# Optimization experiments

Measured on AMD Instinct MI355X. Metric: run time of the kernel, lower is better.

The kernel has to match this reference:

```python
import jax, jax.numpy as jnp
import numpy as np

N_NODES = 50000
N_EDGES = 800000
D_IN = 128
D_OUT = 128


def setup_inputs() -> dict:
    key = jax.random.key(0)
    k1, k2, k3, k4 = jax.random.split(key, 4)
    node_features = jax.random.normal(k1, (N_NODES, D_IN), dtype=jnp.float32)
    edge_index = jax.random.randint(k2, (2, N_EDGES), 0, N_NODES, dtype=jnp.int64)
    # nn.Linear params: weight [out, in], bias [out]
    W = jax.random.normal(k3, (D_OUT, D_IN), dtype=jnp.float32) / np.sqrt(D_IN)
    b = jax.random.normal(k4, (D_OUT,), dtype=jnp.float32) * 0.01
    return {"node_features": node_features, "edge_index": edge_index, "W": W, "b": b}


def reference(node_features, edge_index, W, b):
    source_nodes = edge_index[0]
    dest_nodes = edge_index[1]
    # gather neighbor features [E, D_in], scatter-add into [N, D_in]
    neighbor_features = node_features[source_nodes]
    aggregated = jax.ops.segment_sum(neighbor_features, dest_nodes,
                                     num_segments=node_features.shape[0])
    # nn.Linear: x @ W.T + b
    return aggregated @ W.T + b
```

## Files before the change

### kernel.cpp

```cpp
#include <hip/hip_runtime.h>


constexpr int NN = 50000;
constexpr int NE = 800000;
constexpr int D  = 128;

constexpr int BS   = 128;
constexpr int NB   = (NN + BS - 1) / BS;
constexpr int EPB  = 4096;
constexpr int NSB  = (NE + EPB - 1) / EPB;
constexpr int CAP  = 4096;

constexpr int AROWU = 136;

typedef __attribute__((ext_vector_type(8))) short bf16x8;
typedef __attribute__((ext_vector_type(4))) float f32x4;
typedef __attribute__((ext_vector_type(2))) float f32x2;

__device__ inline unsigned short f2bf(float f) {
    unsigned u = __float_as_uint(f);
    return (unsigned short)((u + 0x7fffu + ((u >> 16) & 1u)) >> 16);
}
__device__ inline float bflo(unsigned v) { return __uint_as_float(v << 16); }
__device__ inline float bfhi(unsigned v) { return __uint_as_float(v & 0xffff0000u); }

__device__ inline int wscan(int v) {
    #pragma unroll
    for (int o = 1; o < 64; o <<= 1) {
        int u = __shfl_up(v, o);
        if ((int)(threadIdx.x & 63) >= o) v += u;
    }
    return v;
}

__device__ inline void acc8(f32x2& a0, f32x2& a1, f32x2& a2, f32x2& a3, uint4 v) {
    a0 += (f32x2){bflo(v.x), bfhi(v.x)};
    a1 += (f32x2){bflo(v.y), bfhi(v.y)};
    a2 += (f32x2){bflo(v.z), bfhi(v.z)};
    a3 += (f32x2){bflo(v.w), bfhi(v.w)};
}

constexpr int NF4 = NN * D / 4;
constexpr int W4  = D * D / 4;
constexpr int NBLK_P = (NF4 + W4 + 511) / 512;
constexpr int GRID_A = NSB + NBLK_P;

__global__ __launch_bounds__(512) void k_prep_bucket(
    const float* __restrict__ nf, const float* __restrict__ W,
    const int* __restrict__ ei,
    ushort* __restrict__ nfh, ushort* __restrict__ Wh,
    ushort* __restrict__ offs, unsigned* __restrict__ buf)
{
    __shared__ int hist[NB], cur[NB];
    __shared__ int wsum[8];
    __shared__ unsigned spk[EPB];
    const int t = threadIdx.x, lane = t & 63, w = t >> 6;

    if (blockIdx.x < NSB) {
        const int blk = blockIdx.x;
        const int e0  = blk * EPB;
        int cnt = NE - e0; if (cnt > EPB) cnt = EPB;

        for (int i = t; i < NB; i += 512) hist[i] = 0;
        __syncthreads();

        unsigned pk[8];
        #pragma unroll
        for (int j = 0; j < 8; ++j) {
            int idx = j * 512 + t;
            if (idx < cnt) {
                int e = e0 + idx;
                unsigned s = (unsigned)ei[e];
                unsigned d = (unsigned)ei[NE + e];
                pk[j] = (d << 16) | s;
                atomicAdd(&hist[pk[j] >> 23], 1);
            }
        }
        __syncthreads();
        int h = (t < NB) ? hist[t] : 0;
        int v = wscan(h);
        if (lane == 63) wsum[w] = v;
        __syncthreads();
        int addv = 0;
        #pragma unroll
        for (int i = 0; i < 8; ++i) addv += (i < w) ? wsum[i] : 0;
        v += addv;
        if (t < NB) {
            int ex = v - h;
            cur[t] = ex;
            offs[t * NSB + blk] = (ushort)ex;
        }
        if (t == 0) offs[NB * NSB + blk] = (ushort)cnt;
        __syncthreads();
        #pragma unroll
        for (int j = 0; j < 8; ++j) {
            int idx = j * 512 + t;
            if (idx < cnt) {
                int l = atomicAdd(&cur[pk[j] >> 23], 1);
                spk[l] = pk[j];
            }
        }
        __syncthreads();
        for (int i = t; i < cnt; i += 512)
            buf[(size_t)blk * EPB + i] = spk[i];
    } else {
        int i = (blockIdx.x - NSB) * 512 + t;
        if (i < NF4) {
            float4 v = ((const float4*)nf)[i];
            ((ushort4*)nfh)[i] = make_ushort4(f2bf(v.x), f2bf(v.y), f2bf(v.z), f2bf(v.w));
        } else if (i < NF4 + W4) {
            int k = i - NF4;
            float4 v = ((const float4*)W)[k];
            ((ushort4*)Wh)[k] = make_ushort4(f2bf(v.x), f2bf(v.y), f2bf(v.z), f2bf(v.w));
        }
    }
}

__global__ __launch_bounds__(1024, 8) void k_sort_agg(
    const unsigned* __restrict__ nfh, const unsigned* __restrict__ buf,
    const ushort* __restrict__ offs, const ushort* __restrict__ Wh,
    const float* __restrict__ bias, float* __restrict__ out)
{
    __shared__ ushort srt[CAP];
    __shared__ int scnt[256];
    __shared__ int sbase[NSB], rbase[NSB];
    __shared__ int hist[BS], off[BS], cur[BS];
    __shared__ int wred[16];
    __shared__ __align__(16) unsigned tile[BS * AROWU / 2];
    const int b = blockIdx.x, t = threadIdx.x;
    const int lane = t & 63, w = t >> 6;

    int my = 0;
    if (t < NSB) {
        int o0 = (int)offs[b * NSB + t];
        int o1 = (int)offs[(b + 1) * NSB + t];
        rbase[t] = o0;
        my = o1 - o0;
    }
    if (t < BS) hist[t] = 0;
    int vs = 0;
    if (w < 4) {
        vs = wscan(my);
        if (lane == 63) wred[w] = vs;
    }
    __syncthreads();
    if (w < 4) {
        int addv = 0;
        #pragma unroll
        for (int i = 0; i < 3; ++i) addv += (i < w) ? wred[i] : 0;
        vs += addv;
        scnt[t] = vs;
        if (t < NSB) sbase[t] = vs - my;
    }
    __syncthreads();
    int total = scnt[NSB - 1];
    if (total > CAP) total = CAP;

    unsigned mypk[4];
    int mycnt = 0;
    #pragma unroll
    for (int j = 0; j < 4; ++j) {
        int p = t + j * 1024;
        if (p < total) {
            int lo = 0, hi = NSB - 1;
            while (lo < hi) {
                int mid = (lo + hi) >> 1;
                if (scnt[mid] > p) hi = mid; else lo = mid + 1;
            }
            unsigned pk = buf[(size_t)lo * EPB + rbase[lo] + (p - sbase[lo])];
            mypk[j] = pk;
            atomicAdd(&hist[(pk >> 16) & (BS - 1)], 1);
            mycnt = j + 1;
        }
    }
    __syncthreads();

    int hv = (t < BS) ? hist[t] : 0;
    int nv = 0;
    if (w < 2) {
        nv = wscan(hv);
        if (lane == 63) wred[8 + w] = nv;
    }
    __syncthreads();
    if (t < BS) {
        int ex = nv + ((w == 1) ? wred[8] : 0) - hv;
        off[t] = ex; cur[t] = ex;
    }
    __syncthreads();
    #pragma unroll
    for (int j = 0; j < 4; ++j) {
        if (j < mycnt) {
            unsigned pk = mypk[j];
            int n = (pk >> 16) & (BS - 1);
            int p = atomicAdd(&cur[n], 1);
            srt[p] = (ushort)(pk & 0xffffu);
        }
    }
    __syncthreads();

    const int qq = lane >> 4;
    const int sl = lane & 15;
    const uint4* nfv = (const uint4*)nfh;

    #pragma unroll 1
    for (int i = 0; i < 2; ++i) {
        const int n = w * 8 + i * 4 + qq;
        const int beg = off[n], cnt = hist[n];
        f32x2 a0 = {0.f, 0.f}, a1 = {0.f, 0.f}, a2 = {0.f, 0.f}, a3 = {0.f, 0.f};
        const int nfull = cnt & ~3;
        if (nfull > 0) {
            uint4 v0 = nfv[(size_t)srt[beg + 0] * 16 + sl];
            uint4 v1 = nfv[(size_t)srt[beg + 1] * 16 + sl];
            uint4 v2 = nfv[(size_t)srt[beg + 2] * 16 + sl];
            uint4 v3 = nfv[(size_t)srt[beg + 3] * 16 + sl];
            for (int p = 4; p < nfull; p += 4) {
                uint4 u0 = nfv[(size_t)srt[beg + p + 0] * 16 + sl];
                uint4 u1 = nfv[(size_t)srt[beg + p + 1] * 16 + sl];
                uint4 u2 = nfv[(size_t)srt[beg + p + 2] * 16 + sl];
                uint4 u3 = nfv[(size_t)srt[beg + p + 3] * 16 + sl];
                acc8(a0, a1, a2, a3, v0);
                acc8(a0, a1, a2, a3, v1);
                acc8(a0, a1, a2, a3, v2);
                acc8(a0, a1, a2, a3, v3);
                v0 = u0; v1 = u1; v2 = u2; v3 = u3;
            }
            acc8(a0, a1, a2, a3, v0);
            acc8(a0, a1, a2, a3, v1);
            acc8(a0, a1, a2, a3, v2);
            acc8(a0, a1, a2, a3, v3);
        }
        const int r = cnt - nfull;
        uint4 t0, t1, t2;
        if (r > 0) t0 = nfv[(size_t)srt[beg + nfull + 0] * 16 + sl];
        if (r > 1) t1 = nfv[(size_t)srt[beg + nfull + 1] * 16 + sl];
        if (r > 2) t2 = nfv[(size_t)srt[beg + nfull + 2] * 16 + sl];
        if (r > 0) acc8(a0, a1, a2, a3, t0);
        if (r > 1) acc8(a0, a1, a2, a3, t1);
        if (r > 2) acc8(a0, a1, a2, a3, t2);

        uint4 o;
        o.x = (unsigned)f2bf(a0.x) | ((unsigned)f2bf(a0.y) << 16);
        o.y = (unsigned)f2bf(a1.x) | ((unsigned)f2bf(a1.y) << 16);
        o.z = (unsigned)f2bf(a2.x) | ((unsigned)f2bf(a2.y) << 16);
        o.w = (unsigned)f2bf(a3.x) | ((unsigned)f2bf(a3.y) << 16);
        *(uint4*)(tile + n * (AROWU / 2) + sl * 4) = o;
    }
    __syncthreads();

    const int m = lane & 15, q = lane >> 4;
    const ushort* lds = (const ushort*)tile;
    #pragma unroll
    for (int i = 0; i < 4; ++i) {
        const int task = w + 16 * i;
        const int t16  = task >> 3;
        const int c0   = (task & 7) * 16;
        const int grow0 = b * BS + t16 * 16;
        if (grow0 < NN) {
            bf16x8 a[4];
            const ushort* arow = lds + (t16 * 16 + m) * AROWU + q * 8;
            #pragma unroll
            for (int kk = 0; kk < 4; ++kk)
                a[kk] = *(const bf16x8*)(arow + kk * 32);
            float bv = bias[c0 + m];
            f32x4 acc = { bv, bv, bv, bv };
            const ushort* wrow = Wh + (size_t)(c0 + m) * D + q * 8;
            #pragma unroll
            for (int kk = 0; kk < 4; ++kk) {
                bf16x8 bb = *(const bf16x8*)(wrow + kk * 32);
                acc = __builtin_amdgcn_mfma_f32_16x16x32_bf16(a[kk], bb, acc, 0, 0, 0);
            }
            float* op = out + (size_t)(grow0 + q * 4) * D + c0 + m;
            op[0]     = acc[0];
            op[D]     = acc[1];
            op[2 * D] = acc[2];
            op[3 * D] = acc[3];
        }
    }
}

extern "C" void kernel_launch(void* const* d_in, const int* in_sizes, int n_in,
                              void* d_out, int out_size, void* d_ws, size_t ws_size,
                              hipStream_t stream) {
    const float* nf = (const float*)d_in[0];
    const int*   ei = (const int*)d_in[1];
    const float* W  = (const float*)d_in[2];
    const float* b  = (const float*)d_in[3];
    float* out = (float*)d_out;

    ushort*   nfh  = (ushort*)d_ws;
    ushort*   Wh   = nfh + (size_t)NN * D;
    unsigned* buf  = (unsigned*)(Wh + D * D);
    ushort*   offs = (ushort*)(buf + (size_t)NSB * EPB);

    k_prep_bucket<<<GRID_A, 512, 0, stream>>>(nf, W, ei, nfh, Wh, offs, buf);
    k_sort_agg   <<<NB, 1024, 0, stream>>>((const unsigned*)nfh, buf, offs, Wh, b, out);
}
```

Measured before the change: 130.9 us.

## Bin edges by source-node quarter so blocks gather in synchronized source ranges

The per-block counting sort now keys on destination node and the top two bits of the source index, giving 512 bins. The gather loop walks the four source quarters in order, keeping accumulators for both destination nodes in registers across quarters. The intent is to make concurrently running waves touch the same quarter of the bf16 feature table at the same time, improving L2/MALL locality for the random gathers. It costs a larger histogram scan, more bins with small counts, and more loop overhead from short remainder tails.

```diff
diff --git a/kernel.cpp b/kernel.cpp
--- a/kernel.cpp
+++ b/kernel.cpp
@@ -10,6 +10,9 @@
 constexpr int EPB  = 4096;
 constexpr int NSB  = (NE + EPB - 1) / EPB;
 constexpr int CAP  = 4096;
+
+constexpr int NQ   = 4;
+constexpr int BINS = BS * NQ;
 
 constexpr int AROWU = 136;
 
@@ -124,7 +127,7 @@
     __shared__ ushort srt[CAP];
     __shared__ int scnt[256];
     __shared__ int sbase[NSB], rbase[NSB];
-    __shared__ int hist[BS], off[BS], cur[BS];
+    __shared__ int hist[BINS], off[BINS], cur[BINS];
     __shared__ int wred[16];
     __shared__ __align__(16) unsigned tile[BS * AROWU / 2];
     const int b = blockIdx.x, t = threadIdx.x;
@@ -137,7 +140,7 @@
         rbase[t] = o0;
         my = o1 - o0;
     }
-    if (t < BS) hist[t] = 0;
+    if (t < BINS) hist[t] = 0;
     int vs = 0;
     if (w < 4) {
         vs = wscan(my);
@@ -169,21 +172,25 @@
             }
             unsigned pk = buf[(size_t)lo * EPB + rbase[lo] + (p - sbase[lo])];
             mypk[j] = pk;
-            atomicAdd(&hist[(pk >> 16) & (BS - 1)], 1);
+            int bin = ((pk >> 16) & (BS - 1)) * NQ + ((pk & 0xffffu) >> 14);
+            atomicAdd(&hist[bin], 1);
             mycnt = j + 1;
         }
     }
     __syncthreads();
 
-    int hv = (t < BS) ? hist[t] : 0;
+    int hv = (t < BINS) ? hist[t] : 0;
     int nv = 0;
-    if (w < 2) {
+    if (w < 8) {
         nv = wscan(hv);
         if (lane == 63) wred[8 + w] = nv;
     }
     __syncthreads();
-    if (t < BS) {
-        int ex = nv + ((w == 1) ? wred[8] : 0) - hv;
+    if (t < BINS) {
+        int addv = 0;
+        #pragma unroll
+        for (int i = 0; i < 7; ++i) addv += (i < w) ? wred[8 + i] : 0;
+        int ex = nv + addv - hv;
         off[t] = ex; cur[t] = ex;
     }
     __syncthreads();
@@ -191,8 +198,8 @@
     for (int j = 0; j < 4; ++j) {
         if (j < mycnt) {
             unsigned pk = mypk[j];
-            int n = (pk >> 16) & (BS - 1);
-            int p = atomicAdd(&cur[n], 1);
+            int bin = ((pk >> 16) & (BS - 1)) * NQ + ((pk & 0xffffu) >> 14);
+            int p = atomicAdd(&cur[bin], 1);
             srt[p] = (ushort)(pk & 0xffffu);
         }
     }
@@ -202,47 +209,61 @@
     const int sl = lane & 15;
     const uint4* nfv = (const uint4*)nfh;
 
+    f32x2 A0[4] = {{0.f,0.f},{0.f,0.f},{0.f,0.f},{0.f,0.f}};
+    f32x2 A1[4] = {{0.f,0.f},{0.f,0.f},{0.f,0.f},{0.f,0.f}};
+
     #pragma unroll 1
-    for (int i = 0; i < 2; ++i) {
-        const int n = w * 8 + i * 4 + qq;
-        const int beg = off[n], cnt = hist[n];
-        f32x2 a0 = {0.f, 0.f}, a1 = {0.f, 0.f}, a2 = {0.f, 0.f}, a3 = {0.f, 0.f};
-        const int nfull = cnt & ~3;
-        if (nfull > 0) {
-            uint4 v0 = nfv[(size_t)srt[beg + 0] * 16 + sl];
-            uint4 v1 = nfv[(size_t)srt[beg + 1] * 16 + sl];
-            uint4 v2 = nfv[(size_t)srt[beg + 2] * 16 + sl];
-            uint4 v3 = nfv[(size_t)srt[beg + 3] * 16 + sl];
-            for (int p = 4; p < nfull; p += 4) {
-                uint4 u0 = nfv[(size_t)srt[beg + p + 0] * 16 + sl];
-                uint4 u1 = nfv[(size_t)srt[beg + p + 1] * 16 + sl];
-                uint4 u2 = nfv[(size_t)srt[beg + p + 2] * 16 + sl];
-                uint4 u3 = nfv[(size_t)srt[beg + p + 3] * 16 + sl];
+    for (int q = 0; q < NQ; ++q) {
+        #pragma unroll
+        for (int i = 0; i < 2; ++i) {
+            const int n = w * 8 + i * 4 + qq;
+            const int bin = n * NQ + q;
+            const int beg = off[bin], cnt = hist[bin];
+            f32x2& a0 = i ? A1[0] : A0[0];
+            f32x2& a1 = i ? A1[1] : A0[1];
+            f32x2& a2 = i ? A1[2] : A0[2];
+            f32x2& a3 = i ? A1[3] : A0[3];
+            const int nfull = cnt & ~3;
+            if (nfull > 0) {
+                uint4 v0 = nfv[(size_t)srt[beg + 0] * 16 + sl];
+                uint4 v1 = nfv[(size_t)srt[beg + 1] * 16 + sl];
+                uint4 v2 = nfv[(size_t)srt[beg + 2] * 16 + sl];
+                uint4 v3 = nfv[(size_t)srt[beg + 3] * 16 + sl];
+                for (int p = 4; p < nfull; p += 4) {
+                    uint4 u0 = nfv[(size_t)srt[beg + p + 0] * 16 + sl];
+                    uint4 u1 = nfv[(size_t)srt[beg + p + 1] * 16 + sl];
+                    uint4 u2 = nfv[(size_t)srt[beg + p + 2] * 16 + sl];
+                    uint4 u3 = nfv[(size_t)srt[beg + p + 3] * 16 + sl];
+                    acc8(a0, a1, a2, a3, v0);
+                    acc8(a0, a1, a2, a3, v1);
+                    acc8(a0, a1, a2, a3, v2);
+                    acc8(a0, a1, a2, a3, v3);
+                    v0 = u0; v1 = u1; v2 = u2; v3 = u3;
+                }
                 acc8(a0, a1, a2, a3, v0);
                 acc8(a0, a1, a2, a3, v1);
                 acc8(a0, a1, a2, a3, v2);
                 acc8(a0, a1, a2, a3, v3);
-                v0 = u0; v1 = u1; v2 = u2; v3 = u3;
-            }
-            acc8(a0, a1, a2, a3, v0);
-            acc8(a0, a1, a2, a3, v1);
-            acc8(a0, a1, a2, a3, v2);
-            acc8(a0, a1, a2, a3, v3);
-        }
-        const int r = cnt - nfull;
-        uint4 t0, t1, t2;
-        if (r > 0) t0 = nfv[(size_t)srt[beg + nfull + 0] * 16 + sl];
-        if (r > 1) t1 = nfv[(size_t)srt[beg + nfull + 1] * 16 + sl];
-        if (r > 2) t2 = nfv[(size_t)srt[beg + nfull + 2] * 16 + sl];
-        if (r > 0) acc8(a0, a1, a2, a3, t0);
-        if (r > 1) acc8(a0, a1, a2, a3, t1);
-        if (r > 2) acc8(a0, a1, a2, a3, t2);
-
+            }
+            const int r = cnt - nfull;
+            uint4 t0, t1, t2;
+            if (r > 0) t0 = nfv[(size_t)srt[beg + nfull + 0] * 16 + sl];
+            if (r > 1) t1 = nfv[(size_t)srt[beg + nfull + 1] * 16 + sl];
+            if (r > 2) t2 = nfv[(size_t)srt[beg + nfull + 2] * 16 + sl];
+            if (r > 0) acc8(a0, a1, a2, a3, t0);
+            if (r > 1) acc8(a0, a1, a2, a3, t1);
+            if (r > 2) acc8(a0, a1, a2, a3, t2);
+        }
+    }
+    #pragma unroll
+    for (int i = 0; i < 2; ++i) {
+        const int n = w * 8 + i * 4 + qq;
+        f32x2* A = i ? A1 : A0;
         uint4 o;
-        o.x = (unsigned)f2bf(a0.x) | ((unsigned)f2bf(a0.y) << 16);
-        o.y = (unsigned)f2bf(a1.x) | ((unsigned)f2bf(a1.y) << 16);
-        o.z = (unsigned)f2bf(a2.x) | ((unsigned)f2bf(a2.y) << 16);
-        o.w = (unsigned)f2bf(a3.x) | ((unsigned)f2bf(a3.y) << 16);
+        o.x = (unsigned)f2bf(A[0].x) | ((unsigned)f2bf(A[0].y) << 16);
+        o.y = (unsigned)f2bf(A[1].x) | ((unsigned)f2bf(A[1].y) << 16);
+        o.z = (unsigned)f2bf(A[2].x) | ((unsigned)f2bf(A[2].y) << 16);
+        o.w = (unsigned)f2bf(A[3].x) | ((unsigned)f2bf(A[3].y) << 16);
         *(uint4*)(tile + n * (AROWU / 2) + sl * 4) = o;
     }
     __syncthreads();
```

Result: slower. 142.6 us (+8.9%).
